# Performance work log

Hardware: AMD Instinct MI355X
Metric: run time of the kernel (lower is better)

Reference implementation:

```python
import jax, jax.numpy as jnp
import numpy as np

B, S, D, H = 2, 2048, 1024, 16
HD = D // H  # head_dim = 64


def setup_inputs() -> dict:
    key = jax.random.key(0)
    ks = jax.random.split(key, 12)
    scale = 1.0 / np.sqrt(D)
    inp = {
        "query": jax.random.normal(ks[0], (B, S, D), dtype=jnp.float32),
        "key_in": jax.random.normal(ks[1], (B, S, D), dtype=jnp.float32),
        "value": jax.random.normal(ks[2], (B, S, D), dtype=jnp.float32),
        "mask": jnp.zeros((B, S), dtype=bool),
        # nn.Linear weights stored as [out, in] like torch; y = x @ W.T + b
        "Wq": jax.random.normal(ks[3], (D, D), dtype=jnp.float32) * scale,
        "bq": jnp.zeros((D,), dtype=jnp.float32),
        "Wk": jax.random.normal(ks[4], (D, D), dtype=jnp.float32) * scale,
        "bk": jnp.zeros((D,), dtype=jnp.float32),
        "Wv": jax.random.normal(ks[5], (D, D), dtype=jnp.float32) * scale,
        "bv": jnp.zeros((D,), dtype=jnp.float32),
        "Wo": jax.random.normal(ks[6], (D, D), dtype=jnp.float32) * scale,
        "bo": jnp.zeros((D,), dtype=jnp.float32),
    }
    return inp


def reference(query, key_in, value, mask, Wq, bq, Wk, bk, Wv, bv, Wo, bo):
    def split_heads(x):  # [B,S,D] -> [B,H,S,HD]
        return x.reshape(B, -1, H, HD).transpose(0, 2, 1, 3)

    Q = split_heads(query @ Wq.T + bq)
    K = split_heads(key_in @ Wk.T + bk)
    V = split_heads(value @ Wv.T + bv)

    scores = jnp.einsum("bhqd,bhkd->bhqk", Q, K) / np.sqrt(HD)
    # key-padding mask: True -> -inf, broadcast over heads and query positions
    scores = jnp.where(mask[:, None, None, :], -jnp.inf, scores)
    attn = jax.nn.softmax(scores, axis=-1)
    out = jnp.einsum("bhqk,bhkd->bhqd", attn, V)  # [B,H,S,HD]
    out = out.transpose(0, 2, 1, 3).reshape(B, -1, D)
    return out @ Wo.T + bo
```

## Files before the change

### kernel.cpp

```cpp
#include <hip/hip_runtime.h>

typedef __attribute__((ext_vector_type(8))) __bf16 bf16x8;
typedef __attribute__((ext_vector_type(4))) float f32x4;
typedef __attribute__((ext_vector_type(16))) float f32x16;
typedef __attribute__((ext_vector_type(4))) unsigned int u32x4;
typedef __attribute__((ext_vector_type(8))) _Float16 f16x8;
typedef __attribute__((ext_vector_type(4))) _Float16 f16x4;
typedef unsigned short us;

#define SEQ 2048
#define DIM 1024
#define NH 16
#define HDIM 64

#define QSCALE 0.1803368801111204f

__device__ inline us f2bf(float f) {
    unsigned u = __builtin_bit_cast(unsigned, f);
    u += 0x7FFFu + ((u >> 16) & 1u);
    return (us)(u >> 16);
}

__device__ inline unsigned sx32(unsigned v) {
    return (unsigned)__shfl_xor((int)v, 32);
}

__device__ __forceinline__ size_t qk_idx(int bh, int s, int d) {
    return (((size_t)bh * 64 + (s >> 5)) << 11) + ((d >> 4) << 9)
         + (((s & 31) + (((d >> 3) & 1) << 5)) << 3) + (d & 7);
}
__device__ __forceinline__ size_t v_idx(int bh, int d, int s) {
    return (((size_t)bh * 64 + (s >> 5)) << 11) + ((((d >> 5) << 1) + ((s >> 4) & 1)) << 9)
         + (((d & 31) + (((s >> 3) & 1) << 5)) << 3) + (s & 7);
}

__device__ __forceinline__ void gload16(const us* g, us* l) {
    __builtin_amdgcn_global_load_lds(
        (const __attribute__((address_space(1))) unsigned int*)(const void*)g,
        (__attribute__((address_space(3))) unsigned int*)(void*)l, 16, 0, 0);
}

__global__ __launch_bounds__(256) void prep(
    const float* __restrict__ q, const float* __restrict__ k, const float* __restrict__ v,
    const float* __restrict__ Wq, const float* __restrict__ Wk,
    const float* __restrict__ Wv, const float* __restrict__ Wo,
    const unsigned char* __restrict__ mask,
    us* __restrict__ acts, us* __restrict__ wts, unsigned* __restrict__ mw)
{
    int bid = blockIdx.x, tid = threadIdx.x;
    if (bid < 12288) {
        int which = bid >> 12;
        const float* src = (which == 0) ? q : (which == 1) ? k : v;
        int i = ((bid & 4095) * 256 + tid) * 4;
        float4 vv = *(const float4*)(src + i);
        ushort4 o;
        o.x = f2bf(vv.x); o.y = f2bf(vv.y); o.z = f2bf(vv.z); o.w = f2bf(vv.w);
        *(ushort4*)(acts + (size_t)which * 4194304 + i) = o;
    } else if (bid < 16384) {
        int wb = bid - 12288;
        int which = wb >> 10;
        const float* src = (which == 0) ? Wq : (which == 1) ? Wk
                         : (which == 2) ? Wv : Wo;
        int i = ((wb & 1023) * 256 + tid) * 4;
        float4 vv = *(const float4*)(src + i);
        ushort4 o;
        o.x = f2bf(vv.x); o.y = f2bf(vv.y); o.z = f2bf(vv.z); o.w = f2bf(vv.w);
        *(ushort4*)(wts + (size_t)which * 1048576 + i) = o;
    } else {
        if (tid < 128) {
            unsigned wv = 0;
#pragma unroll
            for (int j = 0; j < 32; j++) wv |= (mask[tid * 32 + j] ? 1u : 0u) << j;
            mw[tid] = wv;
        }
    }
}

#define BM 128
#define BN 128
#define BK 64

__device__ __forceinline__ void gemm_core(
    const us* __restrict__ A, const us* __restrict__ W,
    const float* __restrict__ bias, void* __restrict__ out,
    int m0, int n0, int mode, float oscale)
{
    __shared__ us lA[BM * BK];
    __shared__ us lB[BN * BK];

    const int tid  = threadIdx.x;
    const int lane = tid & 63;
    const int w    = tid >> 6;
    const int wm   = w >> 1, wn = w & 1;
    const int g    = lane >> 4, li = lane & 15;
    const int K    = DIM, N = DIM;

    const f32x4 fz = {0.f, 0.f, 0.f, 0.f};
    f32x4 acc[4][4];
#pragma unroll
    for (int i = 0; i < 4; i++)
#pragma unroll
        for (int j = 0; j < 4; j++) acc[i][j] = fz;

    for (int k0 = 0; k0 < K; k0 += BK) {
#pragma unroll
        for (int i = 0; i < 4; i++) {
            int v = tid + i * 256;
            int row = v >> 3, c8 = (v & 7) * 8;
            gload16(&A[(size_t)(m0 + row) * K + k0 + c8], &lA[v * 8]);
            gload16(&W[(size_t)(n0 + row) * K + k0 + c8], &lB[v * 8]);
        }
        __syncthreads();
#pragma unroll
        for (int kk = 0; kk < 2; kk++) {
            bf16x8 af[4], bfr[4];
#pragma unroll
            for (int i = 0; i < 4; i++)
                af[i] = *(const bf16x8*)&lA[(wm * 64 + i * 16 + li) * BK + kk * 32 + g * 8];
#pragma unroll
            for (int j = 0; j < 4; j++)
                bfr[j] = *(const bf16x8*)&lB[(wn * 64 + j * 16 + li) * BK + kk * 32 + g * 8];
#pragma unroll
            for (int i = 0; i < 4; i++)
#pragma unroll
                for (int j = 0; j < 4; j++)
                    acc[i][j] = __builtin_amdgcn_mfma_f32_16x16x32_bf16(
                        af[i], bfr[j], acc[i][j], 0, 0, 0);
        }
        __syncthreads();
    }

    const int r0 = g * 4;
#pragma unroll
    for (int i = 0; i < 4; i++) {
#pragma unroll
        for (int j = 0; j < 4; j++) {
            int col = n0 + wn * 64 + j * 16 + li;
            float bs = bias[col];
#pragma unroll
            for (int r = 0; r < 4; r++) {
                int row = m0 + wm * 64 + i * 16 + r0 + r;
                float val = (acc[i][j][r] + bs) * oscale;
                if (mode == 2) {
                    ((float*)out)[(size_t)row * N + col] = val;
                } else {
                    int s = row & (SEQ - 1);
                    int bh = ((row >> 11) << 4) + (col >> 6);
                    int d  = col & (HDIM - 1);
                    size_t idx = (mode == 0) ? qk_idx(bh, s, d) : v_idx(bh, d, s);
                    ((us*)out)[idx] = f2bf(val);
                }
            }
        }
    }
}

__global__ __launch_bounds__(256) void gemm_qkv(
    const us* __restrict__ xq, const us* __restrict__ xk, const us* __restrict__ xv,
    const us* __restrict__ wq, const us* __restrict__ wk, const us* __restrict__ wv,
    const float* __restrict__ bq, const float* __restrict__ bk, const float* __restrict__ bv,
    us* __restrict__ Qb, us* __restrict__ Kb, us* __restrict__ VTb)
{
    int L    = blockIdx.x;
    int orig = (L & 7) * 96 + (L >> 3);
    int z    = orig >> 8;
    int rem  = orig & 255;
    int m0   = (rem >> 3) * BM, n0 = (rem & 7) * BN;
    if (z == 0)      gemm_core(xq, wq, bq, Qb,  m0, n0, 0, QSCALE);
    else if (z == 1) gemm_core(xk, wk, bk, Kb,  m0, n0, 0, 1.0f);
    else             gemm_core(xv, wv, bv, VTb, m0, n0, 1, 1.0f);
}

__global__ __launch_bounds__(256) void gemm_one(
    const us* __restrict__ A, const us* __restrict__ W,
    const float* __restrict__ bias, float* __restrict__ out)
{
    int L    = blockIdx.x;
    int orig = (L & 7) * 32 + (L >> 3);
    int m0   = (orig >> 3) * BM, n0 = (orig & 7) * BN;
    gemm_core(A, W, bias, out, m0, n0, 2, 1.0f);
}

__global__ __launch_bounds__(256, 4) void attn_split(
    const us* __restrict__ Qb, const us* __restrict__ Kb,
    const us* __restrict__ VT, const unsigned* __restrict__ mw,
    _Float16* __restrict__ opart, float* __restrict__ mlpart)
{
    const int tid  = threadIdx.x;
    const int w    = tid >> 6, lane = tid & 63;
    const int unit = blockIdx.x * 4 + w;
    const int tile = unit >> 1, half = unit & 1;
    const int bh   = tile >> 6, qt = tile & 63;
    const int b    = bh >> 4;
    const int q0   = qt * 32;
    const int ql   = lane & 31, hi = lane >> 5;
    const int kv0  = half * 1024, kv1 = kv0 + 1024;

    const us* Qf = Qb + (((size_t)bh * 64 + qt) << 11) + lane * 8;
    const us* Kf = Kb + (((size_t)bh * 64) << 11) + lane * 8;
    const us* Vf = VT + (((size_t)bh * 64) << 11) + lane * 8;

    bf16x8 qf[4];
#pragma unroll
    for (int t = 0; t < 4; t++) qf[t] = *(const bf16x8*)(Qf + t * 512);

    const f32x16 z16 = {0,0,0,0,0,0,0,0,0,0,0,0,0,0,0,0};
    f32x16 o0 = z16, o1 = z16;
    float mrun = -1e30f, lrun = 0.f;

    bf16x8 kf[4];
#pragma unroll
    for (int t = 0; t < 4; t++)
        kf[t] = *(const bf16x8*)(Kf + ((size_t)(kv0 >> 5) << 11) + t * 512);

    for (int kv = kv0; kv < kv1; kv += 32) {
        const size_t koff = (size_t)(kv >> 5) << 11;

        f32x16 s = z16;
#pragma unroll
        for (int t = 0; t < 4; t++)
            s = __builtin_amdgcn_mfma_f32_32x32x16_bf16(kf[t], qf[t], s, 0, 0, 0);

        if (kv + 32 < kv1) {
            const us* Kn = Kf + koff + 2048;
#pragma unroll
            for (int t = 0; t < 4; t++) kf[t] = *(const bf16x8*)(Kn + t * 512);
        }
        bf16x8 vf0[2], vf1[2];
#pragma unroll
        for (int t = 0; t < 2; t++) {
            vf0[t] = *(const bf16x8*)(Vf + koff + t * 512);
            vf1[t] = *(const bf16x8*)(Vf + koff + 1024 + t * 512);
        }

        unsigned m32 = (unsigned)__builtin_amdgcn_readfirstlane(
            (int)mw[b * 64 + (kv >> 5)]);

        float t8[8];
#pragma unroll
        for (int j = 0; j < 8; j++) t8[j] = fmaxf(s[j], s[j + 8]);
#pragma unroll
        for (int j = 0; j < 4; j++) t8[j] = fmaxf(t8[j], t8[j + 4]);
        float pmax = fmaxf(fmaxf(t8[0], t8[1]), fmaxf(t8[2], t8[3]));

        if (!__all(pmax <= mrun + 8.f)) {
            float pm = fmaxf(pmax, __shfl_xor(pmax, 32));
            float nm = fmaxf(mrun, pm);
            float corr = __builtin_amdgcn_exp2f(mrun - nm);
            lrun *= corr;
#pragma unroll
            for (int j = 0; j < 16; j++) { o0[j] *= corr; o1[j] *= corr; }
            mrun = nm;
        }

        float p[16];
#pragma unroll
        for (int r = 0; r < 16; r++) p[r] = __builtin_amdgcn_exp2f(s[r] - mrun);
        if (m32) {
            unsigned ms = hi ? (m32 >> 4) : m32;
#pragma unroll
            for (int r = 0; r < 16; r++)
                if ((ms >> ((r & 3) + 8 * (r >> 2))) & 1) p[r] = 0.f;
        }
        float a8[8];
#pragma unroll
        for (int j = 0; j < 8; j++) a8[j] = p[j] + p[j + 8];
#pragma unroll
        for (int j = 0; j < 4; j++) a8[j] += a8[j + 4];
        lrun += (a8[0] + a8[1]) + (a8[2] + a8[3]);

        unsigned pw[8];
#pragma unroll
        for (int j = 0; j < 8; j++)
            asm("v_cvt_pk_bf16_f32 %0, %1, %2"
                : "=v"(pw[j]) : "v"(p[2 * j]), "v"(p[2 * j + 1]));

        unsigned y0 = sx32(hi ? pw[0] : pw[2]);
        unsigned y1 = sx32(hi ? pw[1] : pw[3]);
        unsigned y2 = sx32(hi ? pw[4] : pw[6]);
        unsigned y3 = sx32(hi ? pw[5] : pw[7]);

        u32x4 t0, t1;
        t0.x = hi ? y0    : pw[0];
        t0.y = hi ? y1    : pw[1];
        t0.z = hi ? pw[2] : y0;
        t0.w = hi ? pw[3] : y1;
        t1.x = hi ? y2    : pw[4];
        t1.y = hi ? y3    : pw[5];
        t1.z = hi ? pw[6] : y2;
        t1.w = hi ? pw[7] : y3;
        bf16x8 pa0 = __builtin_bit_cast(bf16x8, t0);
        bf16x8 pa1 = __builtin_bit_cast(bf16x8, t1);

        o0 = __builtin_amdgcn_mfma_f32_32x32x16_bf16(vf0[0], pa0, o0, 0, 0, 0);
        o0 = __builtin_amdgcn_mfma_f32_32x32x16_bf16(vf0[1], pa1, o0, 0, 0, 0);
        o1 = __builtin_amdgcn_mfma_f32_32x32x16_bf16(vf1[0], pa0, o1, 0, 0, 0);
        o1 = __builtin_amdgcn_mfma_f32_32x32x16_bf16(vf1[1], pa1, o1, 0, 0, 0);
    }

    float lh  = lrun + __shfl_xor(lrun, 32);
    float inv = __builtin_amdgcn_rcpf(lh);

    size_t orow = (size_t)half * 65536 + (size_t)bh * SEQ + q0 + ql;
    _Float16* od = opart + orow * 64;
#pragma unroll
    for (int g2 = 0; g2 < 4; g2++) {
        f16x4 v0, v1;
#pragma unroll
        for (int j = 0; j < 4; j++) {
            v0[j] = (_Float16)(o0[4 * g2 + j] * inv);
            v1[j] = (_Float16)(o1[4 * g2 + j] * inv);
        }
        *(f16x4*)(od + 8 * g2 + 4 * hi)      = v0;
        *(f16x4*)(od + 32 + 8 * g2 + 4 * hi) = v1;
    }
    if (hi == 0) {
        float2 mlv; mlv.x = mrun; mlv.y = lh;
        *(float2*)&mlpart[orow * 2] = mlv;
    }
}

__global__ __launch_bounds__(256) void attn_combine(
    const _Float16* __restrict__ op, const float* __restrict__ ml,
    us* __restrict__ AO)
{
    int t   = blockIdx.x * 256 + threadIdx.x;
    int row = t >> 3, dc = (t & 7) * 8;
    int bh  = row >> 11, q = row & (SEQ - 1);
    int b   = bh >> 4, h = bh & 15;

    float2 ml0 = *(const float2*)&ml[(size_t)row * 2];
    float2 ml1 = *(const float2*)&ml[(size_t)(65536 + row) * 2];
    float M  = fmaxf(ml0.x, ml1.x);
    float w0 = ml0.y * __builtin_amdgcn_exp2f(ml0.x - M);
    float w1 = ml1.y * __builtin_amdgcn_exp2f(ml1.x - M);
    float wi = __builtin_amdgcn_rcpf(w0 + w1);
    float a0 = w0 * wi, a1 = w1 * wi;

    f16x8 v0 = *(const f16x8*)(op + (size_t)row * 64 + dc);
    f16x8 v1 = *(const f16x8*)(op + 4194304 + (size_t)row * 64 + dc);

    ushort4 r0, r1;
    r0.x = f2bf(a0 * (float)v0[0] + a1 * (float)v1[0]);
    r0.y = f2bf(a0 * (float)v0[1] + a1 * (float)v1[1]);
    r0.z = f2bf(a0 * (float)v0[2] + a1 * (float)v1[2]);
    r0.w = f2bf(a0 * (float)v0[3] + a1 * (float)v1[3]);
    r1.x = f2bf(a0 * (float)v0[4] + a1 * (float)v1[4]);
    r1.y = f2bf(a0 * (float)v0[5] + a1 * (float)v1[5]);
    r1.z = f2bf(a0 * (float)v0[6] + a1 * (float)v1[6]);
    r1.w = f2bf(a0 * (float)v0[7] + a1 * (float)v1[7]);

    us* dst = AO + ((size_t)b * SEQ + q) * DIM + h * HDIM + dc;
    *(ushort4*)dst       = r0;
    *(ushort4*)(dst + 4) = r1;
}

extern "C" void kernel_launch(void* const* d_in, const int* in_sizes, int n_in,
                              void* d_out, int out_size, void* d_ws, size_t ws_size,
                              hipStream_t stream)
{
    const float* q  = (const float*)d_in[0];
    const float* k  = (const float*)d_in[1];
    const float* v  = (const float*)d_in[2];
    const unsigned char* mask = (const unsigned char*)d_in[3];
    const float* Wq = (const float*)d_in[4];
    const float* bq = (const float*)d_in[5];
    const float* Wk = (const float*)d_in[6];
    const float* bk = (const float*)d_in[7];
    const float* Wv = (const float*)d_in[8];
    const float* bv = (const float*)d_in[9];
    const float* Wo = (const float*)d_in[10];
    const float* bo = (const float*)d_in[11];

    us* ws  = (us*)d_ws;
    us* xq  = ws;
    us* xk  = ws + 4194304;
    us* xv  = ws + 8388608;
    us* wqb = ws + 12582912;
    us* wkb = ws + 13631488;
    us* wvb = ws + 14680064;
    us* wob = ws + 15728640;
    us* Qb  = ws + 16777216;
    us* Kb  = ws + 20971520;
    us* VTb = ws + 25165824;
    us* AO  = ws + 29360128;
    unsigned* mwords = (unsigned*)(ws + 33554432);
    _Float16* opart  = (_Float16*)ws;
    float*    mlpart = (float*)(ws + 8388608 + 524288);

    prep<<<dim3(16385), 256, 0, stream>>>(q, k, v, Wq, Wk, Wv, Wo, mask,
                                          xq, wqb, mwords);

    gemm_qkv<<<dim3(768), 256, 0, stream>>>(
        xq, xk, xv, wqb, wkb, wvb, bq, bk, bv, Qb, Kb, VTb);

    attn_split<<<dim3(1024), 256, 0, stream>>>(Qb, Kb, VTb, mwords, opart, mlpart);
    attn_combine<<<dim3(2048), 256, 0, stream>>>(opart, mlpart, AO);

    gemm_one<<<dim3(256), 256, 0, stream>>>(AO, wob, bo, (float*)d_out);
}
```

Before: 263.9 us.

## Fuse split-KV attention combine into attention kernel via shared memory

Each block now handles one 32-query tile, with its four waves each covering a quarter of the KV range. The waves' partial outputs and max/sum statistics are merged in LDS and written directly as bf16 into AO. This removes the separate combine kernel launch and the global round trip of the fp16 partials and statistics. It also adds a block-level barrier and LDS usage, raises the launch-bounds occupancy hint to 8, and remaps blocks so neighbouring blocks share the same head.

```diff
diff --git a/kernel.cpp b/kernel.cpp
--- a/kernel.cpp
+++ b/kernel.cpp
@@ -181,20 +181,22 @@
     gemm_core(A, W, bias, out, m0, n0, 2, 1.0f);
 }
 
-__global__ __launch_bounds__(256, 4) void attn_split(
+__global__ __launch_bounds__(256, 8) void attn_fused(
     const us* __restrict__ Qb, const us* __restrict__ Kb,
     const us* __restrict__ VT, const unsigned* __restrict__ mw,
-    _Float16* __restrict__ opart, float* __restrict__ mlpart)
-{
+    us* __restrict__ AO)
+{
+    __shared__ _Float16 lo[4][32][64];
+    __shared__ float    lml[4][32][2];
+
     const int tid  = threadIdx.x;
     const int w    = tid >> 6, lane = tid & 63;
-    const int unit = blockIdx.x * 4 + w;
-    const int tile = unit >> 1, half = unit & 1;
+    const int L    = blockIdx.x;
+    const int tile = (L & 7) * 256 + (L >> 3);
     const int bh   = tile >> 6, qt = tile & 63;
-    const int b    = bh >> 4;
-    const int q0   = qt * 32;
+    const int b    = bh >> 4, h = bh & 15;
     const int ql   = lane & 31, hi = lane >> 5;
-    const int kv0  = half * 1024, kv1 = kv0 + 1024;
+    const int kv0  = w * 512, kv1 = kv0 + 512;
 
     const us* Qf = Qb + (((size_t)bh * 64 + qt) << 11) + lane * 8;
     const us* Kf = Kb + (((size_t)bh * 64) << 11) + lane * 8;
@@ -301,8 +303,7 @@
     float lh  = lrun + __shfl_xor(lrun, 32);
     float inv = __builtin_amdgcn_rcpf(lh);
 
-    size_t orow = (size_t)half * 65536 + (size_t)bh * SEQ + q0 + ql;
-    _Float16* od = opart + orow * 64;
+    _Float16* od = &lo[w][ql][0];
 #pragma unroll
     for (int g2 = 0; g2 < 4; g2++) {
         f16x4 v0, v1;
@@ -314,45 +315,39 @@
         *(f16x4*)(od + 8 * g2 + 4 * hi)      = v0;
         *(f16x4*)(od + 32 + 8 * g2 + 4 * hi) = v1;
     }
-    if (hi == 0) {
-        float2 mlv; mlv.x = mrun; mlv.y = lh;
-        *(float2*)&mlpart[orow * 2] = mlv;
-    }
-}
-
-__global__ __launch_bounds__(256) void attn_combine(
-    const _Float16* __restrict__ op, const float* __restrict__ ml,
-    us* __restrict__ AO)
-{
-    int t   = blockIdx.x * 256 + threadIdx.x;
-    int row = t >> 3, dc = (t & 7) * 8;
-    int bh  = row >> 11, q = row & (SEQ - 1);
-    int b   = bh >> 4, h = bh & 15;
-
-    float2 ml0 = *(const float2*)&ml[(size_t)row * 2];
-    float2 ml1 = *(const float2*)&ml[(size_t)(65536 + row) * 2];
-    float M  = fmaxf(ml0.x, ml1.x);
-    float w0 = ml0.y * __builtin_amdgcn_exp2f(ml0.x - M);
-    float w1 = ml1.y * __builtin_amdgcn_exp2f(ml1.x - M);
-    float wi = __builtin_amdgcn_rcpf(w0 + w1);
-    float a0 = w0 * wi, a1 = w1 * wi;
-
-    f16x8 v0 = *(const f16x8*)(op + (size_t)row * 64 + dc);
-    f16x8 v1 = *(const f16x8*)(op + 4194304 + (size_t)row * 64 + dc);
-
-    ushort4 r0, r1;
-    r0.x = f2bf(a0 * (float)v0[0] + a1 * (float)v1[0]);
-    r0.y = f2bf(a0 * (float)v0[1] + a1 * (float)v1[1]);
-    r0.z = f2bf(a0 * (float)v0[2] + a1 * (float)v1[2]);
-    r0.w = f2bf(a0 * (float)v0[3] + a1 * (float)v1[3]);
-    r1.x = f2bf(a0 * (float)v0[4] + a1 * (float)v1[4]);
-    r1.y = f2bf(a0 * (float)v0[5] + a1 * (float)v1[5]);
-    r1.z = f2bf(a0 * (float)v0[6] + a1 * (float)v1[6]);
-    r1.w = f2bf(a0 * (float)v0[7] + a1 * (float)v1[7]);
-
-    us* dst = AO + ((size_t)b * SEQ + q) * DIM + h * HDIM + dc;
-    *(ushort4*)dst       = r0;
-    *(ushort4*)(dst + 4) = r1;
+    if (hi == 0) { lml[w][ql][0] = mrun; lml[w][ql][1] = lh; }
+    __syncthreads();
+
+    {
+        int qrow = tid >> 3, dc = (tid & 7) * 8;
+        float m0v = lml[0][qrow][0], m1v = lml[1][qrow][0];
+        float m2v = lml[2][qrow][0], m3v = lml[3][qrow][0];
+        float M = fmaxf(fmaxf(m0v, m1v), fmaxf(m2v, m3v));
+        float a0 = lml[0][qrow][1] * __builtin_amdgcn_exp2f(m0v - M);
+        float a1 = lml[1][qrow][1] * __builtin_amdgcn_exp2f(m1v - M);
+        float a2 = lml[2][qrow][1] * __builtin_amdgcn_exp2f(m2v - M);
+        float a3 = lml[3][qrow][1] * __builtin_amdgcn_exp2f(m3v - M);
+        float wi = __builtin_amdgcn_rcpf(a0 + a1 + a2 + a3);
+        a0 *= wi; a1 *= wi; a2 *= wi; a3 *= wi;
+
+        f16x8 p0 = *(const f16x8*)&lo[0][qrow][dc];
+        f16x8 p1 = *(const f16x8*)&lo[1][qrow][dc];
+        f16x8 p2 = *(const f16x8*)&lo[2][qrow][dc];
+        f16x8 p3 = *(const f16x8*)&lo[3][qrow][dc];
+
+        ushort4 r0, r1;
+        float vj[8];
+#pragma unroll
+        for (int j = 0; j < 8; j++)
+            vj[j] = a0 * (float)p0[j] + a1 * (float)p1[j]
+                  + a2 * (float)p2[j] + a3 * (float)p3[j];
+        r0.x = f2bf(vj[0]); r0.y = f2bf(vj[1]); r0.z = f2bf(vj[2]); r0.w = f2bf(vj[3]);
+        r1.x = f2bf(vj[4]); r1.y = f2bf(vj[5]); r1.z = f2bf(vj[6]); r1.w = f2bf(vj[7]);
+
+        us* dst = AO + ((size_t)b * SEQ + qt * 32 + qrow) * DIM + h * HDIM + dc;
+        *(ushort4*)dst       = r0;
+        *(ushort4*)(dst + 4) = r1;
+    }
 }
 
 extern "C" void kernel_launch(void* const* d_in, const int* in_sizes, int n_in,
@@ -385,8 +380,6 @@
     us* VTb = ws + 25165824;
     us* AO  = ws + 29360128;
     unsigned* mwords = (unsigned*)(ws + 33554432);
-    _Float16* opart  = (_Float16*)ws;
-    float*    mlpart = (float*)(ws + 8388608 + 524288);
 
     prep<<<dim3(16385), 256, 0, stream>>>(q, k, v, Wq, Wk, Wv, Wo, mask,
                                           xq, wqb, mwords);
@@ -394,8 +387,7 @@
     gemm_qkv<<<dim3(768), 256, 0, stream>>>(
         xq, xk, xv, wqb, wkb, wvb, bq, bk, bv, Qb, Kb, VTb);
 
-    attn_split<<<dim3(1024), 256, 0, stream>>>(Qb, Kb, VTb, mwords, opart, mlpart);
-    attn_combine<<<dim3(2048), 256, 0, stream>>>(opart, mlpart, AO);
+    attn_fused<<<dim3(2048), 256, 0, stream>>>(Qb, Kb, VTb, mwords, AO);
 
     gemm_one<<<dim3(256), 256, 0, stream>>>(AO, wob, bo, (float*)d_out);
 }
```

Measured after the change: 716.6 us. +171.5%, slower.
